# Kernel tuning notes

Hardware: AMD Instinct MI355X
Metric: run time of the kernel (lower is better)

Reference implementation:

```python
import jax, jax.numpy as jnp
import numpy as np

N = 50000      # nodes
E = 800000     # edges
H, C = 4, 32   # heads, per-head channels
NF = 513       # n_fft//2 + 1 frequency bins
NMEL = 128
NEG_SLOPE_ATT = 0.2   # GATConv leaky_relu slope
NEG_SLOPE_MLP = 0.01  # F.leaky_relu default


def setup_inputs() -> dict:
    key = jax.random.key(0)
    ks = jax.random.split(key, 12)
    s = 0.05
    return {
        "x": jax.random.normal(ks[0], (N, NF), jnp.float32),
        "edge_index": jax.random.randint(ks[1], (2, E), 0, N, dtype=jnp.int32),
        "fb": jax.random.normal(ks[2], (NF, NMEL), jnp.float32) * s,
        "Wg": jax.random.normal(ks[3], (NMEL, H * C), jnp.float32) * s,
        "bias_g": jnp.zeros((H * C,), jnp.float32),
        "att_src": jax.random.normal(ks[4], (H, C), jnp.float32) * s,
        "att_dst": jax.random.normal(ks[5], (H, C), jnp.float32) * s,
        "W1": jax.random.normal(ks[6], (H * C, 256), jnp.float32) * s,
        "b1": jnp.zeros((256,), jnp.float32),
        "W2": jax.random.normal(ks[7], (256, 128), jnp.float32) * s,
        "b2": jnp.zeros((128,), jnp.float32),
        "W3": jax.random.normal(ks[8], (128, 10), jnp.float32) * s,
        "b3": jnp.zeros((10,), jnp.float32),
    }


def gat_conv(h, src, dst, att_src, att_dst, bias_g):
    # h: [N, H, C]; per-edge attention, segment softmax over dst, scatter-add
    a_s = jnp.einsum('nhc,hc->nh', h, att_src)  # [N, H]
    a_d = jnp.einsum('nhc,hc->nh', h, att_dst)  # [N, H]
    e = jax.nn.leaky_relu(a_s[src] + a_d[dst], NEG_SLOPE_ATT)  # [E', H]
    m = jax.ops.segment_max(e, dst, num_segments=N)            # [N, H]
    ex = jnp.exp(e - m[dst])
    denom = jax.ops.segment_sum(ex, dst, num_segments=N)       # [N, H]
    alpha = ex / denom[dst]                                    # [E', H]
    msg = h[src] * alpha[:, :, None]                           # [E', H, C]
    out = jax.ops.segment_sum(msg, dst, num_segments=N)        # [N, H, C]
    return out.reshape(N, H * C) + bias_g


def reference(x, edge_index, fb, Wg, bias_g, att_src, att_dst, W1, b1, W2, b2, W3, b3):
    # learnable mel filterbank projection: [N, NF] -> [N, NMEL]
    x = x @ fb
    # GATConv linear transform, split into heads
    h = (x @ Wg).reshape(N, H, C)
    # add self loops (PyG GATConv default add_self_loops=True)
    loop = jnp.arange(N, dtype=edge_index.dtype)
    src = jnp.concatenate([edge_index[0], loop])
    dst = jnp.concatenate([edge_index[1], loop])
    x = jax.nn.elu(gat_conv(h, src, dst, att_src, att_dst, bias_g))
    # dropout is identity in eval mode
    x = jax.nn.leaky_relu(x @ W1 + b1, NEG_SLOPE_MLP)
    x = jax.nn.leaky_relu(x @ W2 + b2, NEG_SLOPE_MLP)
    x = jax.nn.leaky_relu(x @ W3 + b3, NEG_SLOPE_MLP)
    return jax.nn.softmax(x, axis=-1)
```

## Files before the change

### kernel.cpp

```cpp
#include <hip/hip_runtime.h>
#include <hip/hip_bf16.h>

#define NN 50000
#define EE 800000
#define NFR 513
#define NMEL 128
#define HC 128

typedef __bf16 bf16x8 __attribute__((ext_vector_type(8)));
typedef float floatx4 __attribute__((ext_vector_type(4)));

struct __attribute__((packed, aligned(4))) u4a { unsigned x, y, z, w; };

__device__ __forceinline__ unsigned short f2b(float f) {
    unsigned u = __float_as_uint(f);
    u = (u + 0x7FFFu + ((u >> 16) & 1u)) >> 16;
    return (unsigned short)u;
}
__device__ __forceinline__ unsigned short f2bu(unsigned u) {
    u = (u + 0x7FFFu + ((u >> 16) & 1u)) >> 16;
    return (unsigned short)u;
}
__device__ __forceinline__ float b2f(unsigned short s) {
    return __uint_as_float(((unsigned)s) << 16);
}
__device__ __forceinline__ float lexp(float a) {
    a = a > 0.f ? a : 0.2f * a;
    return __expf(a);
}

__device__ __forceinline__ float ldf(const float* p, long i) { return p[i]; }
__device__ __forceinline__ void stf(float* p, long i, float v) { p[i] = v; }
__device__ __forceinline__ void stf(__hip_bfloat16* p, long i, float v) {
    ((unsigned short*)p)[i] = f2b(v);
}

#define BM 64
#define BN 64
#define BK 16

template<int EPI, typename TA, typename TB, typename TC>
__global__ __launch_bounds__(256) void gemm_k(const TA* __restrict__ A, const TB* __restrict__ B,
                                              TC* __restrict__ C, int M, int Nn, int K,
                                              const float* __restrict__ bias)
{
    __shared__ float As[BK][BM + 4];
    __shared__ float Bs[BK][BN + 4];
    const int t = threadIdx.x;
    const int row0 = blockIdx.x * BM;
    const int col0 = blockIdx.y * BN;
    const int tc = t & 15, tr = t >> 4;
    float acc[4][4] = {};

    for (int kb = 0; kb < K; kb += BK) {
        #pragma unroll
        for (int i = 0; i < 4; ++i) {
            int idx = i * 256 + t;
            int r = idx >> 4, k = idx & 15;
            int gr = row0 + r, gk = kb + k;
            float v = 0.f;
            if (gr < M && gk < K) v = ldf(A, (long)gr * K + gk);
            As[k][r] = v;
        }
        #pragma unroll
        for (int i = 0; i < 4; ++i) {
            int idx = i * 256 + t;
            int c = idx & 63, k = idx >> 6;
            int gk = kb + k, gc = col0 + c;
            float v = 0.f;
            if (gk < K && gc < Nn) v = ldf(B, (long)gk * Nn + gc);
            Bs[k][c] = v;
        }
        __syncthreads();
        #pragma unroll
        for (int kk = 0; kk < BK; ++kk) {
            float4 av = *reinterpret_cast<const float4*>(&As[kk][tr << 2]);
            float4 bv = *reinterpret_cast<const float4*>(&Bs[kk][tc << 2]);
            float a[4] = {av.x, av.y, av.z, av.w};
            float b[4] = {bv.x, bv.y, bv.z, bv.w};
            #pragma unroll
            for (int i = 0; i < 4; ++i)
                #pragma unroll
                for (int j = 0; j < 4; ++j)
                    acc[i][j] += a[i] * b[j];
        }
        __syncthreads();
    }

    #pragma unroll
    for (int i = 0; i < 4; ++i) {
        int gr = row0 + (tr << 2) + i;
        if (gr >= M) continue;
        #pragma unroll
        for (int j = 0; j < 4; ++j) {
            int gc = col0 + (tc << 2) + j;
            if (gc >= Nn) continue;
            float v = acc[i][j];
            if (EPI == 2) {
                stf(C, (long)gc * 544 + gr, v);
            } else {
                if (EPI == 1) { v += bias[gc]; v = v > 0.f ? v : 0.01f * v; }
                stf(C, (long)gr * Nn + gc, v);
            }
        }
    }
}

__global__ void k_trans(const float* __restrict__ in, __hip_bfloat16* __restrict__ outp,
                        int K, int N, int KP)
{
    int id = blockIdx.x * 256 + threadIdx.x;
    if (id >= N * KP) return;
    int n = id / KP, k = id % KP;
    float v = (k < K) ? in[(long)k * N + n] : 0.f;
    ((unsigned short*)outp)[id] = f2b(v);
}

#define PS 40

template<typename T> struct ARegs;
template<> struct ARegs<float> { unsigned v[8]; };
template<> struct ARegs<__hip_bfloat16> { uint4 v; };

__device__ __forceinline__ void loadA_r(const float* __restrict__ A, ARegs<float>& r, int t,
                                        int row0, int M, int K, int kb)
{
    #pragma unroll
    for (int g = 0; g < 2; ++g) {
        int q = g * 256 + t;
        int row = q >> 3, k4 = (q & 7) * 4;
        int gr = row0 + row, gk = kb + k4;
        unsigned f0 = 0, f1 = 0, f2 = 0, f3 = 0;
        if (gr < M) {
            const float* ap = A + (long)gr * K + gk;
            if (gk + 3 < K) {
                u4a u = *reinterpret_cast<const u4a*>(ap);
                f0 = u.x; f1 = u.y; f2 = u.z; f3 = u.w;
            } else {
                if (gk + 0 < K) f0 = __float_as_uint(ap[0]);
                if (gk + 1 < K) f1 = __float_as_uint(ap[1]);
                if (gk + 2 < K) f2 = __float_as_uint(ap[2]);
            }
        }
        r.v[g * 4 + 0] = f0; r.v[g * 4 + 1] = f1;
        r.v[g * 4 + 2] = f2; r.v[g * 4 + 3] = f3;
    }
}

__device__ __forceinline__ void writeA_r(unsigned short* As, const ARegs<float>& r, int t)
{
    #pragma unroll
    for (int g = 0; g < 2; ++g) {
        int q = g * 256 + t;
        int row = q >> 3, k4 = (q & 7) * 4;
        ushort4 pk;
        pk.x = f2bu(r.v[g * 4 + 0]); pk.y = f2bu(r.v[g * 4 + 1]);
        pk.z = f2bu(r.v[g * 4 + 2]); pk.w = f2bu(r.v[g * 4 + 3]);
        *reinterpret_cast<ushort4*>(&As[row * PS + k4]) = pk;
    }
}

__device__ __forceinline__ void loadA_r(const __hip_bfloat16* __restrict__ A, ARegs<__hip_bfloat16>& r,
                                        int t, int row0, int M, int K, int kb)
{
    int row = t >> 2, k8 = (t & 3) * 8;
    int gr = row0 + row;
    uint4 val = make_uint4(0, 0, 0, 0);
    if (gr < M) val = *reinterpret_cast<const uint4*>(A + (long)gr * K + kb + k8);
    r.v = val;
}

__device__ __forceinline__ void writeA_r(unsigned short* As, const ARegs<__hip_bfloat16>& r, int t)
{
    int row = t >> 2, k8 = (t & 3) * 8;
    *reinterpret_cast<uint4*>(&As[row * PS + k8]) = r.v;
}

__device__ __forceinline__ void loadB_r(const __hip_bfloat16* __restrict__ Bt, uint4* bR, int t,
                                        int col0, int Nn, int KB, int kb)
{
    #pragma unroll
    for (int g = 0; g < 2; ++g) {
        int c = g * 256 + t;
        int row = c >> 2, k8 = (c & 3) * 8;
        int gn = col0 + row;
        uint4 val = make_uint4(0, 0, 0, 0);
        if (gn < Nn) val = *reinterpret_cast<const uint4*>(Bt + (long)gn * KB + kb + k8);
        bR[g] = val;
    }
}

__device__ __forceinline__ void writeB_r(unsigned short* Bs, const uint4* bR, int t)
{
    #pragma unroll
    for (int g = 0; g < 2; ++g) {
        int c = g * 256 + t;
        int row = c >> 2, k8 = (c & 3) * 8;
        *reinterpret_cast<uint4*>(&Bs[row * PS + k8]) = bR[g];
    }
}

template<int EPI, typename TA, typename TC>
__global__ __launch_bounds__(256) void mgemm(const TA* __restrict__ A,
                                             const __hip_bfloat16* __restrict__ Bt,
                                             TC* __restrict__ C,
                                             int M, int Nn, int K, int KB,
                                             const float* __restrict__ bias)
{
    __shared__ unsigned short As[2][64 * PS];
    __shared__ unsigned short Bs[2][128 * PS];
    const int t = threadIdx.x;
    const int row0 = blockIdx.x * 64;
    const int col0 = blockIdx.y * 128;
    const int wave = t >> 6, lane = t & 63;
    const int wm = (wave >> 1) * 32, wn = (wave & 1) * 64;
    const int lm = lane & 15, kq = lane >> 4;

    floatx4 acc[2][4];
    #pragma unroll
    for (int i = 0; i < 2; ++i)
        #pragma unroll
        for (int j = 0; j < 4; ++j)
            acc[i][j] = 0.f;

    ARegs<TA> aR;
    uint4 bR[2];
    loadA_r(A, aR, t, row0, M, K, 0);
    loadB_r(Bt, bR, t, col0, Nn, KB, 0);

    const int nIter = KB >> 5;
    int b = 0;
    for (int it = 0; it < nIter; ++it) {
        writeA_r(As[b], aR, t);
        writeB_r(Bs[b], bR, t);
        if (it + 1 < nIter) {
            loadA_r(A, aR, t, row0, M, K, (it + 1) * 32);
            loadB_r(Bt, bR, t, col0, Nn, KB, (it + 1) * 32);
        }
        asm volatile("s_waitcnt lgkmcnt(0)" ::: "memory");
        __builtin_amdgcn_s_barrier();
        __builtin_amdgcn_sched_barrier(0);

        bf16x8 af[2], bf[4];
        #pragma unroll
        for (int i = 0; i < 2; ++i)
            af[i] = *reinterpret_cast<const bf16x8*>(&As[b][(wm + i * 16 + lm) * PS + kq * 8]);
        #pragma unroll
        for (int j = 0; j < 4; ++j)
            bf[j] = *reinterpret_cast<const bf16x8*>(&Bs[b][(wn + j * 16 + lm) * PS + kq * 8]);
        #pragma unroll
        for (int i = 0; i < 2; ++i)
            #pragma unroll
            for (int j = 0; j < 4; ++j)
                acc[i][j] = __builtin_amdgcn_mfma_f32_16x16x32_bf16(af[i], bf[j], acc[i][j], 0, 0, 0);
        b ^= 1;
    }

    #pragma unroll
    for (int i = 0; i < 2; ++i) {
        #pragma unroll
        for (int r = 0; r < 4; ++r) {
            int gr = row0 + wm + i * 16 + kq * 4 + r;
            if (gr >= M) continue;
            #pragma unroll
            for (int j = 0; j < 4; ++j) {
                int gc = col0 + wn + j * 16 + lm;
                float v = acc[i][j][r];
                if (EPI == 1) { v += bias[gc]; v = v > 0.f ? v : 0.01f * v; }
                stf(C, (long)gr * Nn + gc, v);
            }
        }
    }
}

__global__ void k_att(const __hip_bfloat16* __restrict__ h, const float* __restrict__ att_src,
                      const float* __restrict__ att_dst,
                      float* __restrict__ a_s, float* __restrict__ a_d)
{
    int id = blockIdx.x * blockDim.x + threadIdx.x;
    if (id >= NN * 4) return;
    int n = id >> 2, hh = id & 3;
    const unsigned short* hr = (const unsigned short*)(h + (long)n * HC + hh * 32);
    float s1 = 0.f, s2 = 0.f;
    #pragma unroll
    for (int c = 0; c < 32; ++c) {
        float v = b2f(hr[c]);
        s1 += v * att_src[hh * 32 + c];
        s2 += v * att_dst[hh * 32 + c];
    }
    a_s[id] = s1;
    a_d[id] = s2;
}

__global__ void k_hist(const int* __restrict__ ei, int* __restrict__ hist)
{
    int e = blockIdx.x * 256 + threadIdx.x;
    if (e < EE) atomicAdd(&hist[ei[EE + e]], 1);
}

__global__ __launch_bounds__(512) void k_scan1(const int* __restrict__ hist, int* __restrict__ start,
                                               int* __restrict__ aux)
{
    __shared__ int sm[512];
    int t = threadIdx.x, i = blockIdx.x * 512 + t;
    int v = (i < NN) ? hist[i] : 0;
    sm[t] = v;
    __syncthreads();
    for (int off = 1; off < 512; off <<= 1) {
        int x = (t >= off) ? sm[t - off] : 0;
        __syncthreads();
        sm[t] += x;
        __syncthreads();
    }
    if (i < NN) start[i] = sm[t] - v;
    if (t == 511) aux[blockIdx.x] = sm[511];
}

__global__ void k_scan2(int* __restrict__ aux, int nb)
{
    if (blockIdx.x == 0 && threadIdx.x == 0) {
        int run = 0;
        for (int b = 0; b < nb; ++b) { int v = aux[b]; aux[b] = run; run += v; }
    }
}

__global__ __launch_bounds__(512) void k_scan3(int* __restrict__ start, int* __restrict__ cursor,
                                               const int* __restrict__ aux)
{
    int i = blockIdx.x * 512 + threadIdx.x;
    if (i < NN) {
        int v = start[i] + aux[blockIdx.x];
        start[i] = v;
        cursor[i] = v;
    }
    if (i == 0) start[NN] = EE;
}

__global__ void k_fill(const int* __restrict__ ei, int* __restrict__ cursor, int* __restrict__ sorted)
{
    int e = blockIdx.x * 256 + threadIdx.x;
    if (e >= EE) return;
    int s = ei[e], d = ei[EE + e];
    int pos = atomicAdd(&cursor[d], 1);
    sorted[pos] = s;
}

__global__ __launch_bounds__(256) void k_agg(const int* __restrict__ start, const int* __restrict__ sorted,
                                             const float* __restrict__ a_s, const float* __restrict__ a_d,
                                             const __hip_bfloat16* __restrict__ h,
                                             const float* __restrict__ bias_g,
                                             __hip_bfloat16* __restrict__ agg)
{
    int wave = threadIdx.x >> 6;
    int lane = threadIdx.x & 63;
    int d = blockIdx.x * 4 + wave;
    if (d >= NN) return;
    int hh = lane >> 4;
    float ad = a_d[d * 4 + hh];
    int e0 = start[d], e1 = start[d + 1];

    float ex = lexp(a_s[d * 4 + hh] + ad);
    unsigned hv = *reinterpret_cast<const unsigned*>(h + (long)d * HC + 2 * lane);
    float acc0 = ex * __uint_as_float(hv << 16);
    float acc1 = ex * __uint_as_float(hv & 0xffff0000u);
    float dsum = ex;

    int e = e0;
    for (; e + 4 <= e1; e += 4) {
        int s0 = sorted[e + 0], s1 = sorted[e + 1], s2 = sorted[e + 2], s3 = sorted[e + 3];
        float as0 = a_s[s0 * 4 + hh], as1 = a_s[s1 * 4 + hh];
        float as2 = a_s[s2 * 4 + hh], as3 = a_s[s3 * 4 + hh];
        unsigned h0 = *reinterpret_cast<const unsigned*>(h + (long)s0 * HC + 2 * lane);
        unsigned h1 = *reinterpret_cast<const unsigned*>(h + (long)s1 * HC + 2 * lane);
        unsigned h2 = *reinterpret_cast<const unsigned*>(h + (long)s2 * HC + 2 * lane);
        unsigned h3 = *reinterpret_cast<const unsigned*>(h + (long)s3 * HC + 2 * lane);
        float x0 = lexp(as0 + ad), x1 = lexp(as1 + ad), x2 = lexp(as2 + ad), x3 = lexp(as3 + ad);
        acc0 += x0 * __uint_as_float(h0 << 16);
        acc1 += x0 * __uint_as_float(h0 & 0xffff0000u);
        acc0 += x1 * __uint_as_float(h1 << 16);
        acc1 += x1 * __uint_as_float(h1 & 0xffff0000u);
        acc0 += x2 * __uint_as_float(h2 << 16);
        acc1 += x2 * __uint_as_float(h2 & 0xffff0000u);
        acc0 += x3 * __uint_as_float(h3 << 16);
        acc1 += x3 * __uint_as_float(h3 & 0xffff0000u);
        dsum += x0 + x1 + x2 + x3;
    }
    for (; e < e1; ++e) {
        int s = sorted[e];
        float xe = lexp(a_s[s * 4 + hh] + ad);
        unsigned hs = *reinterpret_cast<const unsigned*>(h + (long)s * HC + 2 * lane);
        acc0 += xe * __uint_as_float(hs << 16);
        acc1 += xe * __uint_as_float(hs & 0xffff0000u);
        dsum += xe;
    }

    float inv = 1.f / dsum;
    float2 bg = *reinterpret_cast<const float2*>(bias_g + 2 * lane);
    float v0 = acc0 * inv + bg.x;
    float v1 = acc1 * inv + bg.y;
    v0 = v0 > 0.f ? v0 : expm1f(v0);
    v1 = v1 > 0.f ? v1 : expm1f(v1);
    unsigned pk = (unsigned)f2b(v0) | ((unsigned)f2b(v1) << 16);
    *reinterpret_cast<unsigned*>((unsigned short*)agg + (long)d * HC + 2 * lane) = pk;
}

__global__ __launch_bounds__(256) void k_final(const __hip_bfloat16* __restrict__ x2, const float* __restrict__ W3,
                                               const float* __restrict__ b3, float* __restrict__ out)
{
    __shared__ float w3s[128 * 10];
    __shared__ float b3s[10];
    int t = threadIdx.x;
    for (int i = t; i < 128 * 10; i += 256) w3s[i] = W3[i];
    if (t < 10) b3s[t] = b3[t];
    __syncthreads();
    int n = blockIdx.x * 256 + t;
    if (n >= NN) return;

    float l[10];
    #pragma unroll
    for (int j = 0; j < 10; ++j) l[j] = b3s[j];
    const uint4* row = reinterpret_cast<const uint4*>(x2 + (long)n * 128);
    #pragma unroll 4
    for (int c8 = 0; c8 < 16; ++c8) {
        uint4 v = row[c8];
        const unsigned w[4] = {v.x, v.y, v.z, v.w};
        #pragma unroll
        for (int u = 0; u < 4; ++u) {
            float f0 = __uint_as_float(w[u] << 16);
            float f1 = __uint_as_float(w[u] & 0xffff0000u);
            const float* wr = &w3s[(c8 * 8 + u * 2) * 10];
            #pragma unroll
            for (int j = 0; j < 10; ++j) l[j] += f0 * wr[j] + f1 * wr[10 + j];
        }
    }
    float m = -1e30f;
    #pragma unroll
    for (int j = 0; j < 10; ++j) {
        float v = l[j];
        v = v > 0.f ? v : 0.01f * v;
        l[j] = v;
        m = fmaxf(m, v);
    }
    float sum = 0.f;
    #pragma unroll
    for (int j = 0; j < 10; ++j) { l[j] = __expf(l[j] - m); sum += l[j]; }
    float inv = 1.f / sum;
    #pragma unroll
    for (int j = 0; j < 10; ++j) out[(long)n * 10 + j] = l[j] * inv;
}

extern "C" void kernel_launch(void* const* d_in, const int* in_sizes, int n_in,
                              void* d_out, int out_size, void* d_ws, size_t ws_size,
                              hipStream_t stream)
{
    const float* x       = (const float*)d_in[0];
    const int*   ei      = (const int*)d_in[1];
    const float* fb      = (const float*)d_in[2];
    const float* Wg      = (const float*)d_in[3];
    const float* bias_g  = (const float*)d_in[4];
    const float* att_src = (const float*)d_in[5];
    const float* att_dst = (const float*)d_in[6];
    const float* W1      = (const float*)d_in[7];
    const float* b1      = (const float*)d_in[8];
    const float* W2      = (const float*)d_in[9];
    const float* b2      = (const float*)d_in[10];
    const float* W3      = (const float*)d_in[11];
    const float* b3      = (const float*)d_in[12];
    float* out = (float*)d_out;
    float* ws = (float*)d_ws;

    float* a_s = ws + 0;
    float* a_d = ws + 200000;
    __hip_bfloat16* fbWgT = (__hip_bfloat16*)(ws + 400000);
    __hip_bfloat16* W1T   = (__hip_bfloat16*)(ws + 434816);
    __hip_bfloat16* W2T   = (__hip_bfloat16*)(ws + 451200);
    int* hist   = (int*)(ws + 467584);
    int* startA = (int*)(ws + 517584);
    int* aux    = (int*)(ws + 567588);
    int* sorted = (int*)(ws + 567720);
    __hip_bfloat16* hbufB = (__hip_bfloat16*)(ws + 1367720);
    __hip_bfloat16* aggB  = (__hip_bfloat16*)(ws + 4567720);
    __hip_bfloat16* x1B   = (__hip_bfloat16*)(ws + 7767720);
    int* cursor = hist;
    __hip_bfloat16* x2B = hbufB;
    if (ws_size < (size_t)14167720 * sizeof(float)) return;

    hipMemsetAsync(ws + 400000, 0, (size_t)117584 * sizeof(float), stream);

    gemm_k<2, float, float, __hip_bfloat16><<<dim3(9, 2), 256, 0, stream>>>(fb, Wg, fbWgT, NFR, HC, NMEL, nullptr);
    k_trans<<<128, 256, 0, stream>>>(W1, W1T, 128, 256, 128);
    k_trans<<<128, 256, 0, stream>>>(W2, W2T, 256, 128, 256);

    mgemm<0, float, __hip_bfloat16><<<dim3(782, 1), 256, 0, stream>>>(x, fbWgT, hbufB, NN, HC, NFR, 544, nullptr);

    k_att<<<(NN * 4 + 255) / 256, 256, 0, stream>>>(hbufB, att_src, att_dst, a_s, a_d);

    k_hist<<<(EE + 255) / 256, 256, 0, stream>>>(ei, hist);
    k_scan1<<<98, 512, 0, stream>>>(hist, startA, aux);
    k_scan2<<<1, 64, 0, stream>>>(aux, 98);
    k_scan3<<<98, 512, 0, stream>>>(startA, cursor, aux);
    k_fill<<<(EE + 255) / 256, 256, 0, stream>>>(ei, cursor, sorted);

    k_agg<<<(NN + 3) / 4, 256, 0, stream>>>(startA, sorted, a_s, a_d, hbufB, bias_g, aggB);

    mgemm<1, __hip_bfloat16, __hip_bfloat16><<<dim3(782, 2), 256, 0, stream>>>(aggB, W1T, x1B, NN, 256, 128, 128, b1);

    mgemm<1, __hip_bfloat16, __hip_bfloat16><<<dim3(782, 1), 256, 0, stream>>>(x1B, W2T, x2B, NN, 128, 256, 256, b2);

    k_final<<<(NN + 255) / 256, 256, 0, stream>>>(x2B, W3, b3, out);
}
```

Before: 432.3 us.

## Fuse attention scores into first GEMM and final layer into second MLP GEMM

```diff
diff --git a/kernel.cpp b/kernel.cpp
--- a/kernel.cpp
+++ b/kernel.cpp
@@ -205,16 +205,27 @@
                                              const __hip_bfloat16* __restrict__ Bt,
                                              TC* __restrict__ C,
                                              int M, int Nn, int K, int KB,
-                                             const float* __restrict__ bias)
+                                             const float* __restrict__ bias,
+                                             const float* __restrict__ pf1,
+                                             const float* __restrict__ pf2,
+                                             float* __restrict__ po1,
+                                             float* __restrict__ po2)
 {
     __shared__ unsigned short As[2][64 * PS];
     __shared__ unsigned short Bs[2][128 * PS];
+    __shared__ unsigned short x2s[(EPI == 3) ? 64 * 130 : 2];
+    __shared__ float w3s[(EPI == 3) ? 1280 : 1];
+
     const int t = threadIdx.x;
     const int row0 = blockIdx.x * 64;
     const int col0 = blockIdx.y * 128;
     const int wave = t >> 6, lane = t & 63;
     const int wm = (wave >> 1) * 32, wn = (wave & 1) * 64;
     const int lm = lane & 15, kq = lane >> 4;
+
+    if (EPI == 3) {
+        for (int i = t; i < 1280; i += 256) w3s[i] = pf1[i];
+    }
 
     floatx4 acc[2][4];
     #pragma unroll
@@ -260,36 +271,87 @@
     for (int i = 0; i < 2; ++i) {
         #pragma unroll
         for (int r = 0; r < 4; ++r) {
-            int gr = row0 + wm + i * 16 + kq * 4 + r;
+            int lrow = wm + i * 16 + kq * 4 + r;
+            int gr = row0 + lrow;
             if (gr >= M) continue;
             #pragma unroll
             for (int j = 0; j < 4; ++j) {
                 int gc = col0 + wn + j * 16 + lm;
                 float v = acc[i][j][r];
-                if (EPI == 1) { v += bias[gc]; v = v > 0.f ? v : 0.01f * v; }
-                stf(C, (long)gr * Nn + gc, v);
+                if (EPI == 1 || EPI == 3) { v += bias[gc]; v = v > 0.f ? v : 0.01f * v; }
+                if (EPI == 3) x2s[lrow * 130 + gc] = f2b(v);
+                else stf(C, (long)gr * Nn + gc, v);
             }
         }
     }
-}
-
-__global__ void k_att(const __hip_bfloat16* __restrict__ h, const float* __restrict__ att_src,
-                      const float* __restrict__ att_dst,
-                      float* __restrict__ a_s, float* __restrict__ a_d)
-{
-    int id = blockIdx.x * blockDim.x + threadIdx.x;
-    if (id >= NN * 4) return;
-    int n = id >> 2, hh = id & 3;
-    const unsigned short* hr = (const unsigned short*)(h + (long)n * HC + hh * 32);
-    float s1 = 0.f, s2 = 0.f;
-    #pragma unroll
-    for (int c = 0; c < 32; ++c) {
-        float v = b2f(hr[c]);
-        s1 += v * att_src[hh * 32 + c];
-        s2 += v * att_dst[hh * 32 + c];
-    }
-    a_s[id] = s1;
-    a_d[id] = s2;
+
+    if (EPI == 4) {
+        float wsv[4], wdv[4];
+        #pragma unroll
+        for (int j = 0; j < 4; ++j) {
+            int gc = wn + j * 16 + lm;
+            wsv[j] = pf1[gc];
+            wdv[j] = pf2[gc];
+        }
+        #pragma unroll
+        for (int i = 0; i < 2; ++i) {
+            #pragma unroll
+            for (int r = 0; r < 4; ++r) {
+                float s0 = acc[i][0][r] * wsv[0] + acc[i][1][r] * wsv[1];
+                float s1 = acc[i][2][r] * wsv[2] + acc[i][3][r] * wsv[3];
+                float d0 = acc[i][0][r] * wdv[0] + acc[i][1][r] * wdv[1];
+                float d1 = acc[i][2][r] * wdv[2] + acc[i][3][r] * wdv[3];
+                #pragma unroll
+                for (int m = 1; m < 16; m <<= 1) {
+                    s0 += __shfl_xor(s0, m); s1 += __shfl_xor(s1, m);
+                    d0 += __shfl_xor(d0, m); d1 += __shfl_xor(d1, m);
+                }
+                if (lm == 0) {
+                    int grow = row0 + wm + i * 16 + kq * 4 + r;
+                    if (grow < M) {
+                        int h0 = wn >> 5;
+                        po1[grow * 4 + h0]     = s0;
+                        po1[grow * 4 + h0 + 1] = s1;
+                        po2[grow * 4 + h0]     = d0;
+                        po2[grow * 4 + h0 + 1] = d1;
+                    }
+                }
+            }
+        }
+    }
+
+    if (EPI == 3) {
+        __syncthreads();
+        if (t < 64) {
+            int grow = row0 + t;
+            if (grow < M) {
+                float l[10];
+                #pragma unroll
+                for (int j = 0; j < 10; ++j) l[j] = pf2[j];
+                #pragma unroll 8
+                for (int c = 0; c < 128; ++c) {
+                    float xv = b2f(x2s[t * 130 + c]);
+                    const float* wr = &w3s[c * 10];
+                    #pragma unroll
+                    for (int j = 0; j < 10; ++j) l[j] += xv * wr[j];
+                }
+                float m = -1e30f;
+                #pragma unroll
+                for (int j = 0; j < 10; ++j) {
+                    float v = l[j];
+                    v = v > 0.f ? v : 0.01f * v;
+                    l[j] = v;
+                    m = fmaxf(m, v);
+                }
+                float sum = 0.f;
+                #pragma unroll
+                for (int j = 0; j < 10; ++j) { l[j] = __expf(l[j] - m); sum += l[j]; }
+                float inv = 1.f / sum;
+                #pragma unroll
+                for (int j = 0; j < 10; ++j) po1[(long)grow * 10 + j] = l[j] * inv;
+            }
+        }
+    }
 }
 
 __global__ void k_hist(const int* __restrict__ ei, int* __restrict__ hist)
@@ -318,10 +380,18 @@
 
 __global__ void k_scan2(int* __restrict__ aux, int nb)
 {
-    if (blockIdx.x == 0 && threadIdx.x == 0) {
-        int run = 0;
-        for (int b = 0; b < nb; ++b) { int v = aux[b]; aux[b] = run; run += v; }
-    }
+    int l = threadIdx.x;
+    int v0 = (l < nb) ? aux[l] : 0;
+    int v1 = (64 + l < nb) ? aux[64 + l] : 0;
+    int s0 = v0, s1 = v1;
+    for (int off = 1; off < 64; off <<= 1) {
+        int u0 = __shfl_up(s0, off);
+        int u1 = __shfl_up(s1, off);
+        if (l >= off) { s0 += u0; s1 += u1; }
+    }
+    int tot0 = __shfl(s0, 63);
+    if (l < nb) aux[l] = s0 - v0;
+    if (64 + l < nb) aux[64 + l] = tot0 + s1 - v1;
 }
 
 __global__ __launch_bounds__(512) void k_scan3(int* __restrict__ start, int* __restrict__ cursor,
@@ -404,51 +474,6 @@
     *reinterpret_cast<unsigned*>((unsigned short*)agg + (long)d * HC + 2 * lane) = pk;
 }
 
-__global__ __launch_bounds__(256) void k_final(const __hip_bfloat16* __restrict__ x2, const float* __restrict__ W3,
-                                               const float* __restrict__ b3, float* __restrict__ out)
-{
-    __shared__ float w3s[128 * 10];
-    __shared__ float b3s[10];
-    int t = threadIdx.x;
-    for (int i = t; i < 128 * 10; i += 256) w3s[i] = W3[i];
-    if (t < 10) b3s[t] = b3[t];
-    __syncthreads();
-    int n = blockIdx.x * 256 + t;
-    if (n >= NN) return;
-
-    float l[10];
-    #pragma unroll
-    for (int j = 0; j < 10; ++j) l[j] = b3s[j];
-    const uint4* row = reinterpret_cast<const uint4*>(x2 + (long)n * 128);
-    #pragma unroll 4
-    for (int c8 = 0; c8 < 16; ++c8) {
-        uint4 v = row[c8];
-        const unsigned w[4] = {v.x, v.y, v.z, v.w};
-        #pragma unroll
-        for (int u = 0; u < 4; ++u) {
-            float f0 = __uint_as_float(w[u] << 16);
-            float f1 = __uint_as_float(w[u] & 0xffff0000u);
-            const float* wr = &w3s[(c8 * 8 + u * 2) * 10];
-            #pragma unroll
-            for (int j = 0; j < 10; ++j) l[j] += f0 * wr[j] + f1 * wr[10 + j];
-        }
-    }
-    float m = -1e30f;
-    #pragma unroll
-    for (int j = 0; j < 10; ++j) {
-        float v = l[j];
-        v = v > 0.f ? v : 0.01f * v;
-        l[j] = v;
-        m = fmaxf(m, v);
-    }
-    float sum = 0.f;
-    #pragma unroll
-    for (int j = 0; j < 10; ++j) { l[j] = __expf(l[j] - m); sum += l[j]; }
-    float inv = 1.f / sum;
-    #pragma unroll
-    for (int j = 0; j < 10; ++j) out[(long)n * 10 + j] = l[j] * inv;
-}
-
 extern "C" void kernel_launch(void* const* d_in, const int* in_sizes, int n_in,
                               void* d_out, int out_size, void* d_ws, size_t ws_size,
                               hipStream_t stream)
@@ -491,9 +516,8 @@
     k_trans<<<128, 256, 0, stream>>>(W1, W1T, 128, 256, 128);
     k_trans<<<128, 256, 0, stream>>>(W2, W2T, 256, 128, 256);
 
-    mgemm<0, float, __hip_bfloat16><<<dim3(782, 1), 256, 0, stream>>>(x, fbWgT, hbufB, NN, HC, NFR, 544, nullptr);
-
-    k_att<<<(NN * 4 + 255) / 256, 256, 0, stream>>>(hbufB, att_src, att_dst, a_s, a_d);
+    mgemm<4, float, __hip_bfloat16><<<dim3(782, 1), 256, 0, stream>>>(
+        x, fbWgT, hbufB, NN, HC, NFR, 544, nullptr, att_src, att_dst, a_s, a_d);
 
     k_hist<<<(EE + 255) / 256, 256, 0, stream>>>(ei, hist);
     k_scan1<<<98, 512, 0, stream>>>(hist, startA, aux);
@@ -503,9 +527,9 @@
 
     k_agg<<<(NN + 3) / 4, 256, 0, stream>>>(startA, sorted, a_s, a_d, hbufB, bias_g, aggB);
 
-    mgemm<1, __hip_bfloat16, __hip_bfloat16><<<dim3(782, 2), 256, 0, stream>>>(aggB, W1T, x1B, NN, 256, 128, 128, b1);
-
-    mgemm<1, __hip_bfloat16, __hip_bfloat16><<<dim3(782, 1), 256, 0, stream>>>(x1B, W2T, x2B, NN, 128, 256, 256, b2);
-
-    k_final<<<(NN + 255) / 256, 256, 0, stream>>>(x2B, W3, b3, out);
-}
+    mgemm<1, __hip_bfloat16, __hip_bfloat16><<<dim3(782, 2), 256, 0, stream>>>(
+        aggB, W1T, x1B, NN, 256, 128, 128, b1, nullptr, nullptr, nullptr, nullptr);
+
+    mgemm<3, __hip_bfloat16, __hip_bfloat16><<<dim3(782, 1), 256, 0, stream>>>(
+        x1B, W2T, x2B, NN, 128, 256, 256, b2, W3, b3, out, nullptr);
+}
```

Measured after the change: 408.9 us. 5.4% less time.
